# Performance work log

Hardware: AMD Instinct MI355X
Metric: run time of the kernel (lower is better)

The kernel has to match this reference:

```python
import jax, jax.numpy as jnp
import numpy as np

NS = (256, 256, 256)  # voxel grid resolution (Ns init kwarg)
LS = 2.0              # physical extent (Ls init kwarg)
N_PTS = 16777216      # 16M query points


def setup_inputs() -> dict:
    key = jax.random.key(0)
    k1, k2 = jax.random.split(key)
    x = jax.random.normal(k1, (N_PTS, 3), dtype=jnp.float32)  # points in ~[-1,1]
    f = jax.random.normal(k2, NS, dtype=jnp.float32)          # learned voxel grid param
    return {"x": x, "f": f}


def reference(x, f):
    # remap: (pts + 1) / hs[0], hs = Ls / (Ns - 1)  (cubic grid -> scalar h)
    ns_f = jnp.asarray(f.shape, dtype=jnp.float32)  # [3]
    h = LS / (ns_f[0] - 1.0)
    sh = x.shape
    pts = (x.reshape(-1, sh[-1]) + 1.0) / h         # [N,3] grid coords
    # per-dim clamp to [0, Ns_i - 1] in float, then truncate-cast (values >= 0 so trunc == floor)
    idx = jnp.clip(pts, 0.0, ns_f - 1.0).astype(jnp.int32)
    out = f[idx[:, 0], idx[:, 1], idx[:, 2]]        # fused multi-dim gather
    return out.reshape(sh[:-1])
```

## Files before the change

kernel.cpp:

```cpp
#include <hip/hip_runtime.h>


typedef float f32x4 __attribute__((ext_vector_type(4)));

__device__ __forceinline__ int vox_idx(float v) {
    const float h = 2.0f / 255.0f;
    float p = (v + 1.0f) / h;
    p = fminf(fmaxf(p, 0.0f), 255.0f);
    return (int)p;
}

__global__ __launch_bounds__(256) void voxel_gather_kernel(
    const float* __restrict__ x, const float* __restrict__ f,
    float* __restrict__ out, int n16)
{
    int t = blockIdx.x * blockDim.x + threadIdx.x;
    if (t >= n16) return;

    const f32x4* x4 = (const f32x4*)x;
    f32x4 xv[12];
#pragma unroll
    for (int j = 0; j < 12; ++j)
        xv[j] = __builtin_nontemporal_load(&x4[12 * t + j]);

    const float* c = (const float*)xv;
    int idx[16];
#pragma unroll
    for (int k = 0; k < 16; ++k)
        idx[k] = (vox_idx(c[3 * k + 0]) << 16) |
                 (vox_idx(c[3 * k + 1]) << 8) |
                  vox_idx(c[3 * k + 2]);

    f32x4 o[4];
    float* ov = (float*)o;
#pragma unroll
    for (int k = 0; k < 16; ++k)
        ov[k] = f[idx[k]];

#pragma unroll
    for (int j = 0; j < 4; ++j)
        __builtin_nontemporal_store(o[j], &((f32x4*)out)[4 * t + j]);
}

extern "C" void kernel_launch(void* const* d_in, const int* in_sizes, int n_in,
                              void* d_out, int out_size, void* d_ws, size_t ws_size,
                              hipStream_t stream) {
    const float* x = (const float*)d_in[0];
    const float* f = (const float*)d_in[1];
    float* out = (float*)d_out;

    int n = in_sizes[0] / 3;
    int n16 = n / 16;
    dim3 block(256);
    dim3 grid((n16 + block.x - 1) / block.x);
    voxel_gather_kernel<<<grid, block, 0, stream>>>(x, f, out, n16);
}
```

Measured before the change: 531.5 us.

## Stage point coordinates through LDS for coalesced loads and stores

Each block now loads its contiguous slab of coordinates with fully coalesced float4 loads into shared memory, then each thread reads strided points from LDS, computes voxel indices, gathers and writes scalar outputs coalesced across the block. Points per thread drop from 16 to 8, which raises the grid size. The aim is to replace the per-thread strided 192-byte loads with wavefront-contiguous accesses and to spread gathers over more waves. In exchange it adds a barrier, 24KB of LDS per block that may limit occupancy, possible LDS bank conflicts on the stride-3 reads, and scalar rather than vector stores.

```diff
diff --git a/kernel.cpp b/kernel.cpp
--- a/kernel.cpp
+++ b/kernel.cpp
@@ -10,36 +10,46 @@
     return (int)p;
 }
 
+#define P 8
+#define BLK 256
+#define PTS_PER_BLK (P * BLK)
+#define F4_PER_BLK (PTS_PER_BLK * 3 / 4)
+
 __global__ __launch_bounds__(256) void voxel_gather_kernel(
     const float* __restrict__ x, const float* __restrict__ f,
-    float* __restrict__ out, int n16)
+    float* __restrict__ out)
 {
-    int t = blockIdx.x * blockDim.x + threadIdx.x;
-    if (t >= n16) return;
+    __shared__ float lds[PTS_PER_BLK * 3];
 
-    const f32x4* x4 = (const f32x4*)x;
-    f32x4 xv[12];
+    const int tid = threadIdx.x;
+    const long long blk = blockIdx.x;
+
+    const f32x4* x4 = (const f32x4*)x + blk * F4_PER_BLK;
 #pragma unroll
-    for (int j = 0; j < 12; ++j)
-        xv[j] = __builtin_nontemporal_load(&x4[12 * t + j]);
+    for (int j = 0; j < 6; ++j) {
+        f32x4 v = __builtin_nontemporal_load(&x4[tid + BLK * j]);
+        ((f32x4*)lds)[tid + BLK * j] = v;
+    }
+    __syncthreads();
 
-    const float* c = (const float*)xv;
-    int idx[16];
+    int idx[P];
 #pragma unroll
-    for (int k = 0; k < 16; ++k)
-        idx[k] = (vox_idx(c[3 * k + 0]) << 16) |
-                 (vox_idx(c[3 * k + 1]) << 8) |
-                  vox_idx(c[3 * k + 2]);
+    for (int j = 0; j < P; ++j) {
+        int p = tid + BLK * j;
+        float cx = lds[3 * p + 0];
+        float cy = lds[3 * p + 1];
+        float cz = lds[3 * p + 2];
+        idx[j] = (vox_idx(cx) << 16) | (vox_idx(cy) << 8) | vox_idx(cz);
+    }
 
-    f32x4 o[4];
-    float* ov = (float*)o;
+    float r[P];
 #pragma unroll
-    for (int k = 0; k < 16; ++k)
-        ov[k] = f[idx[k]];
+    for (int j = 0; j < P; ++j) r[j] = f[idx[j]];
 
+    float* ob = out + blk * PTS_PER_BLK;
 #pragma unroll
-    for (int j = 0; j < 4; ++j)
-        __builtin_nontemporal_store(o[j], &((f32x4*)out)[4 * t + j]);
+    for (int j = 0; j < P; ++j)
+        __builtin_nontemporal_store(r[j], &ob[tid + BLK * j]);
 }
 
 extern "C" void kernel_launch(void* const* d_in, const int* in_sizes, int n_in,
@@ -50,8 +60,6 @@
     float* out = (float*)d_out;
 
     int n = in_sizes[0] / 3;
-    int n16 = n / 16;
-    dim3 block(256);
-    dim3 grid((n16 + block.x - 1) / block.x);
-    voxel_gather_kernel<<<grid, block, 0, stream>>>(x, f, out, n16);
+    int nblk = n / PTS_PER_BLK;
+    voxel_gather_kernel<<<dim3(nblk), dim3(BLK), 0, stream>>>(x, f, out);
 }
```

New measurement: 429.8 us. 1.24x faster.
